# Optimization experiments

Measured on AMD Instinct MI355X. Metric: run time of the kernel, lower is better.

Reference implementation:

```python
import jax, jax.numpy as jnp
import numpy as np

B, D, Q, U = 4096, 512, 16384, 256  # batch, feat dim, CQ size, unique pids per batch
OIM_SCALAR = 30.0
IGNORE = -1


def _normalize(x):
    # F.normalize(dim=-1): divide by L2 norm clamped to eps
    n = jnp.maximum(jnp.linalg.norm(x, axis=-1, keepdims=True), 1e-12)
    return x / n


def setup_inputs() -> dict:
    key = jax.random.key(0)
    k1, k2, k3 = jax.random.split(key, 3)
    inputs = jax.random.normal(k1, (B, D), dtype=jnp.float32)
    # exactly U unique pids, each repeated B//U times, shuffled
    labels = jax.random.permutation(k2, jnp.arange(B, dtype=jnp.int32) % U)
    emb_cq = jax.random.normal(k3, (Q, D), dtype=jnp.float32)
    emb_cq = _normalize(emb_cq)  # queue stores normalized embeddings
    # unique queue labels; slice overlaps batch pids -> exercises the c==1 branch
    label_cq = jnp.arange(Q, dtype=jnp.int32) + 1000
    label_cq = label_cq.at[5000:5000 + U].set(jnp.arange(U, dtype=jnp.int32))
    age_cq = jnp.ones((Q,), dtype=jnp.int32)
    return {"inputs": inputs, "labels": labels, "emb_cq": emb_cq,
            "label_cq": label_cq, "age_cq": age_cq, "header_cq": 0}


def reference(inputs, labels, emb_cq, label_cq, age_cq, header_cq):
    # ---- per-pid masked mean (torch.unique loop, vectorized) ----
    uniq = jnp.unique(labels, size=U)                      # sorted unique pids [U]
    m_u = (uniq[:, None] == labels[None, :]).astype(inputs.dtype)  # [U,B]
    uniq_emb = (m_u @ inputs) / m_u.sum(axis=1, keepdims=True)     # [U,D]

    inputs_n = _normalize(inputs)
    uniq_emb_n = jax.lax.stop_gradient(_normalize(uniq_emb))  # queue write is under no_grad

    # ---- circular queue update (sequential, data-dependent) ----
    age_cq = age_cq + (label_cq != IGNORE).astype(age_cq.dtype)

    def step(carry, xy):
        emb, lab, age, h = carry
        x, y = xy
        m = lab == y
        c = m.any()
        i = jnp.argmax(m)          # existing slot for pid y (if any)
        emb = emb.at[h].set(x)
        lab = lab.at[h].set(y)
        age = age.at[h].set(1)
        inval = c & (i != h)       # invalidate stale slot
        lab = lab.at[i].set(jnp.where(inval, IGNORE, lab[i]))
        age = age.at[i].set(jnp.where(inval, 0, age[i]))
        return (emb, lab, age, (h + 1) % Q), None

    h0 = jnp.asarray(header_cq, dtype=jnp.int32)
    (emb_cq, label_cq, age_cq, _), _ = jax.lax.scan(
        step, (emb_cq, label_cq, age_cq, h0), (uniq_emb_n, uniq))
    emb_cq = jax.lax.stop_gradient(emb_cq)  # buffer: no grad through the queue

    # ---- cosine-sim cross-entropy over valid queue entries ----
    good = label_cq != IGNORE                               # [Q]
    # each batch pid matches exactly one good queue slot
    xe = jnp.argmax((labels[:, None] == label_cq[None, :]) & good[None, :], axis=1)
    logits = OIM_SCALAR * (inputs_n @ emb_cq.T)             # [B,Q]
    logits = jnp.where(good[None, :], logits, -jnp.inf)     # mask == compacting emb_cq[good]
    logp = jax.nn.log_softmax(logits, axis=1)
    loss = -jnp.mean(logp[jnp.arange(B), xe])               # sum(xe_i)/B
    return loss
```

## Files before the change

kernel.cpp:

```cpp
#include <hip/hip_runtime.h>
#include <hip/hip_bf16.h>

#define Bn 4096
#define Dn 512
#define Qn 16384
#define Un 256
#define OIM 30.0f


typedef int i32x4 __attribute__((ext_vector_type(4)));

__device__ __forceinline__ void async_copy16(const int4* g, int4* l) {
    __builtin_amdgcn_global_load_lds((const __attribute__((address_space(1))) void*)g,
                                     (__attribute__((address_space(3))) void*)l, 16, 0, 0);
}

__device__ __forceinline__ int clamp8(float v, float qs) {
    int q = __float2int_rn(v * qs);
    return max(-127, min(127, q));
}

__global__ void prep_kernel(const float* __restrict__ inputs, const int* __restrict__ labels,
                            const float* __restrict__ emb_cq, const int* __restrict__ label_cq,
                            const int* __restrict__ header,
                            char* __restrict__ inA8, char* __restrict__ embQ8,
                            float* __restrict__ invA, float* __restrict__ invB,
                            float* __restrict__ goodf, float* __restrict__ rowsum,
                            float* __restrict__ out) {
    __shared__ float wred[4];
    __shared__ float wmax[4];
    __shared__ int lidx[64];
    __shared__ int lcnt;
    int blk = blockIdx.x;
    int tid = threadIdx.x;
    float2 o;
    bool isA;
    int drow;
    if (blk == 0 && tid == 0) out[0] = 0.f;
    if (blk < Bn) {
        if (tid == 0) rowsum[blk] = 0.f;
        float2 v = ((const float2*)(inputs + (size_t)blk * Dn))[tid];
        float ss = v.x * v.x + v.y * v.y;
        for (int d = 1; d < 64; d <<= 1) ss += __shfl_xor(ss, d, 64);
        if ((tid & 63) == 0) wred[tid >> 6] = ss;
        __syncthreads();
        float sc = 1.0f / fmaxf(sqrtf(wred[0] + wred[1] + wred[2] + wred[3]), 1e-12f);
        o.x = v.x * sc; o.y = v.y * sc;
        isA = true; drow = blk;
    } else {
        int j = blk - Bn;
        int h0 = header[0];
        int t = j - h0; if (t < 0) t += Qn;
        if (t < Un) {
            if (tid == 0) lcnt = 0;
            __syncthreads();
            for (int b = tid; b < Bn; b += 256)
                if (labels[b] == t) { int s = atomicAdd(&lcnt, 1); if (s < 64) lidx[s] = b; }
            __syncthreads();
            int c = lcnt; if (c > 64) c = 64;
            float2 acc = {0.f, 0.f};
            for (int s = 0; s < c; ++s) {
                float2 x = ((const float2*)(inputs + (size_t)lidx[s] * Dn))[tid];
                acc.x += x.x; acc.y += x.y;
            }
            float inv = 1.0f / (float)(c > 0 ? c : 1);
            acc.x *= inv; acc.y *= inv;
            float ss = acc.x * acc.x + acc.y * acc.y;
            for (int d = 1; d < 64; d <<= 1) ss += __shfl_xor(ss, d, 64);
            if ((tid & 63) == 0) wred[tid >> 6] = ss;
            __syncthreads();
            float sc = 1.0f / fmaxf(sqrtf(wred[0] + wred[1] + wred[2] + wred[3]), 1e-12f);
            o.x = acc.x * sc; o.y = acc.y * sc;
        } else {
            o = ((const float2*)(emb_cq + (size_t)j * Dn))[tid];
        }
        if (tid == 0) {
            int vl = label_cq[j];
            int fin = (vl >= 0 && vl < Un) ? -1 : vl;
            if (t < Un) fin = t;
            goodf[j] = (fin != -1) ? 1.0f : 0.0f;
        }
        isA = false; drow = blk - Bn;
    }
    float am = fmaxf(fabsf(o.x), fabsf(o.y));
    for (int d = 1; d < 64; d <<= 1) am = fmaxf(am, __shfl_xor(am, d, 64));
    if ((tid & 63) == 0) wmax[tid >> 6] = am;
    __syncthreads();
    float m = fmaxf(fmaxf(fmaxf(wmax[0], wmax[1]), fmaxf(wmax[2], wmax[3])), 1e-12f);
    float qs = 127.0f / m;
    char2 pc;
    pc.x = (char)clamp8(o.x, qs);
    pc.y = (char)clamp8(o.y, qs);
    if (isA) {
        int kb = tid * 2;
        size_t addr = (size_t)(drow >> 4) * 8192 + (size_t)(kb >> 4) * 256
                    + (drow & 15) * 16 + (kb & 15);
        *(char2*)(inA8 + addr) = pc;
        if (tid == 0) invA[drow] = m / 127.0f;
    } else {
        *(char2*)(embQ8 + (size_t)drow * Dn + tid * 2) = pc;
        if (tid == 0) invB[drow] = m / 127.0f;
    }
}

__global__ __launch_bounds__(256, 4) void gemm_kernel(
    const char* __restrict__ inA8,
    const char* __restrict__ embQ8,
    const float* __restrict__ invA,
    const float* __restrict__ invB,
    const float* __restrict__ goodf,
    const int* __restrict__ labels,
    const int* __restrict__ header,
    float* __restrict__ rowsum,
    float* __restrict__ target)
{
    const float LOG2E = 1.4426950408889634f;
    const float LN2   = 0.6931471805599453f;
    __shared__ char Bs[4 * 128 * 64];
    __shared__ float rsl[128];
    __shared__ int tgtc[128];
    __shared__ float sAl[128];
    __shared__ float2 sBL[128];
    int tid = threadIdx.x;
    int lane = tid & 63, w = tid >> 6;
    int wm = w >> 1, wn = w & 1;
    int lid = blockIdx.y * gridDim.x + blockIdx.x;
    int xcd = lid & 7, pos = lid >> 3;
    int n0 = (xcd * 16 + (pos & 15)) * 128;
    int m0 = (pos >> 4) * 128;
    if (tid < 128) {
        rsl[tid] = 0.f;
        int tc = header[0] + labels[m0 + tid];
        if (tc >= Qn) tc -= Qn;
        tgtc[tid] = tc;
        sAl[tid] = invA[m0 + tid];
        float2 sb;
        sb.x = invB[n0 + tid];
        sb.y = (goodf[n0 + tid] != 0.f) ? 0.f : -10000.f;
        sBL[tid] = sb;
    }
    i32x4 acc[4][4] = {};
    const int4* Bg = (const int4*)(embQ8 + (size_t)n0 * Dn);
    int4* Bs4 = (int4*)Bs;
    int goff[2];
    #pragma unroll
    for (int t = 0; t < 2; ++t) {
        int g = t * 256 + tid;
        int r = g >> 2, sc = g & 3;
        int c = (sc - (r >> 1)) & 3;
        goff[t] = r * 32 + c;
    }
    int q = lane >> 4;
    int offB[4];
    #pragma unroll
    for (int j = 0; j < 4; ++j) {
        int br = wn * 64 + j * 16 + (lane & 15);
        offB[j] = br * 64 + (((q + (br >> 1)) & 3) << 4);
    }
    const char* Ap[4];
    #pragma unroll
    for (int i = 0; i < 4; ++i)
        Ap[i] = inA8 + (size_t)((m0 >> 4) + wm * 4 + i) * 8192 + lane * 16;
    auto stage2 = [&](int t) {
        int s0 = (t & 3) * 512, s1 = ((t + 1) & 3) * 512;
        #pragma unroll
        for (int u = 0; u < 2; ++u) {
            int g = u * 256 + tid;
            async_copy16(&Bg[goff[u] + t * 4],       &Bs4[s0 + g]);
            async_copy16(&Bg[goff[u] + (t + 1) * 4], &Bs4[s1 + g]);
        }
    };
    i32x4 a0[4], a1[4];
    auto loadA = [&](i32x4* a, int t) {
        #pragma unroll
        for (int i = 0; i < 4; ++i) a[i] = *(const i32x4*)(Ap[i] + t * 1024);
    };
    auto compute = [&](int t, i32x4* a) {
        const char* Bb = Bs + (t & 3) * 8192;
        i32x4 bfr[4];
        #pragma unroll
        for (int j = 0; j < 4; ++j) bfr[j] = *(const i32x4*)(Bb + offB[j]);
        #pragma unroll
        for (int i = 0; i < 4; ++i)
            #pragma unroll
            for (int j = 0; j < 4; ++j)
                acc[i][j] = __builtin_amdgcn_mfma_i32_16x16x64_i8(bfr[j], a[i], acc[i][j], 0, 0, 0);
    };
    stage2(0);
    loadA(a0, 0);
    #pragma unroll
    for (int ww = 0; ww < 8; ww += 2) {
        if (ww == 0)
            asm volatile("s_waitcnt vmcnt(4) lgkmcnt(0)\ns_barrier" ::: "memory");
        else
            asm volatile("s_waitcnt vmcnt(4)\ns_barrier" ::: "memory");
        loadA(a1, ww + 1);
        __builtin_amdgcn_sched_barrier(0);
        if (ww < 6) stage2(ww + 2);
        compute(ww, a0);
        if (ww < 6) loadA(a0, ww + 2);
        compute(ww + 1, a1);
    }
    int bl = lane & 15;
    float2 sbv[16];
    #pragma unroll
    for (int j = 0; j < 4; ++j)
        #pragma unroll
        for (int r = 0; r < 4; ++r)
            sbv[j * 4 + r] = sBL[wn * 64 + j * 16 + q * 4 + r];
    #pragma unroll
    for (int i = 0; i < 4; ++i) {
        int rowl = wm * 64 + i * 16 + bl;
        float fA = (OIM * LOG2E) * sAl[rowl];
        int tc = tgtc[rowl];
        float s = 0.f;
        #pragma unroll
        for (int j = 0; j < 4; ++j) {
            #pragma unroll
            for (int r = 0; r < 4; ++r) {
                int qloc = wn * 64 + j * 16 + q * 4 + r;
                float2 sb = sbv[j * 4 + r];
                float v2 = fA * sb.x * (float)acc[i][j][r] + sb.y;
                s += __builtin_amdgcn_exp2f(v2);
                if (tc == n0 + qloc) target[m0 + rowl] = v2 * LN2;
            }
        }
        s += __shfl_xor(s, 16, 64);
        s += __shfl_xor(s, 32, 64);
        if (q == 0) atomicAdd(&rsl[rowl], s);
    }
    __syncthreads();
    if (tid < 128) atomicAdd(&rowsum[m0 + tid], rsl[tid]);
}

__global__ void loss_kernel(const float* __restrict__ rowsum, const float* __restrict__ target,
                            float* __restrict__ out) {
    __shared__ float red[4];
    int tid = threadIdx.x;
    int b = blockIdx.x * 256 + tid;
    float s = logf(rowsum[b]) - target[b];
    #pragma unroll
    for (int d = 1; d < 64; d <<= 1) s += __shfl_xor(s, d, 64);
    if ((tid & 63) == 0) red[tid >> 6] = s;
    __syncthreads();
    if (tid == 0)
        atomicAdd(out, (red[0] + red[1] + red[2] + red[3]) * (1.0f / (float)Bn));
}

extern "C" void kernel_launch(void* const* d_in, const int* in_sizes, int n_in,
                              void* d_out, int out_size, void* d_ws, size_t ws_size,
                              hipStream_t stream) {
    const float* inputs   = (const float*)d_in[0];
    const int*   labels   = (const int*)d_in[1];
    const float* emb_cq   = (const float*)d_in[2];
    const int*   label_cq = (const int*)d_in[3];
    const int*   header   = (const int*)d_in[5];

    char* ws = (char*)d_ws;
    size_t off = 0;
    auto alloc = [&](size_t bytes) { char* p = ws + off; off += (bytes + 255) & ~(size_t)255; return p; };
    char*  inA8   = (char*)alloc((size_t)Bn * Dn);
    char*  embQ8  = (char*)alloc((size_t)Qn * Dn);
    float* invA   = (float*)alloc(Bn * 4);
    float* invB   = (float*)alloc(Qn * 4);
    float* goodf  = (float*)alloc(Qn * 4);
    float* rowsum = (float*)alloc(Bn * 4);
    float* target = (float*)alloc(Bn * 4);

    hipLaunchKernelGGL(prep_kernel, dim3(Bn + Qn), dim3(256), 0, stream,
                       inputs, labels, emb_cq, label_cq, header,
                       inA8, embQ8, invA, invB, goodf, rowsum, (float*)d_out);
    hipLaunchKernelGGL(gemm_kernel, dim3(Qn / 128, Bn / 128), dim3(256), 0, stream,
                       inA8, embQ8, invA, invB, goodf, labels, header, rowsum, target);
    hipLaunchKernelGGL(loss_kernel, dim3(Bn / 256), dim3(256), 0, stream,
                       rowsum, target, (float*)d_out);
}
```

Measured before the change: 169.9 us.

## Enlarge GEMM tile to 256x256 with 512 threads and 3-stage LDS pipeline

The int8 logits GEMM moves from 128x128 tiles with 256 threads to 256x256 tiles with 512 threads. The queue tile goes through a 3-slot LDS ring buffer with hand-tuned waitcnt values. MFMAs are issued in interleaved pairs under s_setprio, and LDS fragment loads are spread between MFMA groups. The goal is to halve global and LDS traffic per MFMA and hide load latency better. The cost is occupancy dropping to one block per CU, more accumulator registers, and a fused exp/target epilogue restructured around the new wave layout.

```diff
diff --git a/kernel.cpp b/kernel.cpp
--- a/kernel.cpp
+++ b/kernel.cpp
@@ -103,7 +103,46 @@
     }
 }
 
-__global__ __launch_bounds__(256, 4) void gemm_kernel(
+#define LDQ(T, K) (*(const i32x4*)(Bs + ((T) % 3) * 16384 + offQ[K]))
+#define STAGE2(T) do { int _sl = ((T) % 3) * 1024;                         \
+    async_copy16(&Bq[goff0 + (T) * 4], &Bs4[_sl + tid]);                   \
+    async_copy16(&Bq[goff1 + (T) * 4], &Bs4[_sl + 512 + tid]); } while (0)
+
+#define MFMA_PAIR(I0, I1, QA, QB, AF) do {                                 \
+    __builtin_amdgcn_s_setprio(1);                                         \
+    _Pragma("unroll")                                                      \
+    for (int j = 0; j < 4; ++j) {                                          \
+        acc[I0][j] = __builtin_amdgcn_mfma_i32_16x16x64_i8(QA, AF[j], acc[I0][j], 0, 0, 0); \
+        acc[I1][j] = __builtin_amdgcn_mfma_i32_16x16x64_i8(QB, AF[j], acc[I1][j], 0, 0, 0); \
+    }                                                                      \
+    __builtin_amdgcn_s_setprio(0);                                         \
+    __builtin_amdgcn_sched_barrier(0); } while (0)
+
+#define BODY(T, AFC, AFN) do {                                             \
+    __builtin_amdgcn_sched_barrier(0);                                     \
+    if ((T) == 0)      asm volatile("s_waitcnt vmcnt(2) lgkmcnt(0)");      \
+    else if ((T) <= 6) asm volatile("s_waitcnt vmcnt(6)");                 \
+    else               asm volatile("s_waitcnt vmcnt(4)");                 \
+    __builtin_amdgcn_s_barrier();                                          \
+    __builtin_amdgcn_sched_barrier(0);                                     \
+    i32x4 qA = LDQ(T, 0), qB = LDQ(T, 1);                                  \
+    if ((T) < 7) {                                                         \
+        _Pragma("unroll")                                                  \
+        for (int j = 0; j < 4; ++j)                                        \
+            AFN[j] = *(const i32x4*)(Ap[j] + ((T) + 1) * 1024);            \
+    }                                                                      \
+    __builtin_amdgcn_sched_barrier(0);                                     \
+    if ((T) < 6) STAGE2((T) + 2);                                          \
+    __builtin_amdgcn_sched_barrier(0);                                     \
+    i32x4 qC = LDQ(T, 2), qD = LDQ(T, 3);                                  \
+    MFMA_PAIR(0, 1, qA, qB, AFC);                                          \
+    i32x4 qE = LDQ(T, 4), qF = LDQ(T, 5);                                  \
+    MFMA_PAIR(2, 3, qC, qD, AFC);                                          \
+    i32x4 qG = LDQ(T, 6), qH = LDQ(T, 7);                                  \
+    MFMA_PAIR(4, 5, qE, qF, AFC);                                          \
+    MFMA_PAIR(6, 7, qG, qH, AFC); } while (0)
+
+__global__ __launch_bounds__(512, 1) void gemm_kernel(
     const char* __restrict__ inA8,
     const char* __restrict__ embQ8,
     const float* __restrict__ invA,
@@ -116,121 +155,94 @@
 {
     const float LOG2E = 1.4426950408889634f;
     const float LN2   = 0.6931471805599453f;
-    __shared__ char Bs[4 * 128 * 64];
-    __shared__ float rsl[128];
-    __shared__ int tgtc[128];
-    __shared__ float sAl[128];
-    __shared__ float2 sBL[128];
+    __shared__ char Bs[3 * 16384];
+    __shared__ float rsl[256];
+    __shared__ int tgt[256];
+    __shared__ float sAl[256];
+    __shared__ float2 sBL[256];
     int tid = threadIdx.x;
     int lane = tid & 63, w = tid >> 6;
-    int wm = w >> 1, wn = w & 1;
+    int wm = w >> 2, wn = w & 3;
     int lid = blockIdx.y * gridDim.x + blockIdx.x;
     int xcd = lid & 7, pos = lid >> 3;
-    int n0 = (xcd * 16 + (pos & 15)) * 128;
-    int m0 = (pos >> 4) * 128;
-    if (tid < 128) {
+    int q0 = (xcd * 8 + (pos & 7)) * 256;
+    int b0 = (pos >> 3) * 256;
+    if (tid < 256) {
         rsl[tid] = 0.f;
-        int tc = header[0] + labels[m0 + tid];
+        int tc = header[0] + labels[b0 + tid];
         if (tc >= Qn) tc -= Qn;
-        tgtc[tid] = tc;
-        sAl[tid] = invA[m0 + tid];
+        tgt[tid] = tc;
+        sAl[tid] = invA[b0 + tid];
         float2 sb;
-        sb.x = invB[n0 + tid];
-        sb.y = (goodf[n0 + tid] != 0.f) ? 0.f : -10000.f;
+        sb.x = invB[q0 + tid];
+        sb.y = (goodf[q0 + tid] != 0.f) ? 0.f : -10000.f;
         sBL[tid] = sb;
     }
-    i32x4 acc[4][4] = {};
-    const int4* Bg = (const int4*)(embQ8 + (size_t)n0 * Dn);
+    i32x4 acc[8][4] = {};
+    const int4* Bq = (const int4*)(embQ8 + (size_t)q0 * Dn);
     int4* Bs4 = (int4*)Bs;
-    int goff[2];
-    #pragma unroll
-    for (int t = 0; t < 2; ++t) {
-        int g = t * 256 + tid;
-        int r = g >> 2, sc = g & 3;
-        int c = (sc - (r >> 1)) & 3;
-        goff[t] = r * 32 + c;
-    }
-    int q = lane >> 4;
-    int offB[4];
+    int r0 = tid >> 2, sc0 = tid & 3;
+    int goff0 = r0 * 32 + ((sc0 - (r0 >> 1)) & 3);
+    int r1 = 128 + (tid >> 2);
+    int goff1 = r1 * 32 + ((sc0 - (r1 >> 1)) & 3);
+    int qq = lane >> 4;
+    int offQ[8];
+    #pragma unroll
+    for (int i = 0; i < 8; ++i) {
+        int r = wm * 128 + i * 16 + (lane & 15);
+        offQ[i] = r * 64 + (((qq + (r >> 1)) & 3) << 4);
+    }
+    const char* Ap[4];
+    #pragma unroll
+    for (int j = 0; j < 4; ++j)
+        Ap[j] = inA8 + (size_t)((b0 >> 4) + wn * 4 + j) * 8192 + lane * 16;
+    i32x4 af0[4], af1[4];
+    #pragma unroll
+    for (int j = 0; j < 4; ++j) af0[j] = *(const i32x4*)(Ap[j]);
+    __builtin_amdgcn_sched_barrier(0);
+    STAGE2(0);
+    STAGE2(1);
+    BODY(0, af0, af1);
+    BODY(1, af1, af0);
+    BODY(2, af0, af1);
+    BODY(3, af1, af0);
+    BODY(4, af0, af1);
+    BODY(5, af1, af0);
+    BODY(6, af0, af1);
+    BODY(7, af1, af0);
+    int bl = lane & 15;
+    float fAj[4]; int tcj[4]; float sj[4];
     #pragma unroll
     for (int j = 0; j < 4; ++j) {
-        int br = wn * 64 + j * 16 + (lane & 15);
-        offB[j] = br * 64 + (((q + (br >> 1)) & 3) << 4);
-    }
-    const char* Ap[4];
-    #pragma unroll
-    for (int i = 0; i < 4; ++i)
-        Ap[i] = inA8 + (size_t)((m0 >> 4) + wm * 4 + i) * 8192 + lane * 16;
-    auto stage2 = [&](int t) {
-        int s0 = (t & 3) * 512, s1 = ((t + 1) & 3) * 512;
+        int bcol = wn * 64 + j * 16 + bl;
+        fAj[j] = (OIM * LOG2E) * sAl[bcol];
+        tcj[j] = tgt[bcol];
+        sj[j] = 0.f;
+    }
+    #pragma unroll
+    for (int i = 0; i < 8; ++i) {
         #pragma unroll
-        for (int u = 0; u < 2; ++u) {
-            int g = u * 256 + tid;
-            async_copy16(&Bg[goff[u] + t * 4],       &Bs4[s0 + g]);
-            async_copy16(&Bg[goff[u] + (t + 1) * 4], &Bs4[s1 + g]);
-        }
-    };
-    i32x4 a0[4], a1[4];
-    auto loadA = [&](i32x4* a, int t) {
-        #pragma unroll
-        for (int i = 0; i < 4; ++i) a[i] = *(const i32x4*)(Ap[i] + t * 1024);
-    };
-    auto compute = [&](int t, i32x4* a) {
-        const char* Bb = Bs + (t & 3) * 8192;
-        i32x4 bfr[4];
-        #pragma unroll
-        for (int j = 0; j < 4; ++j) bfr[j] = *(const i32x4*)(Bb + offB[j]);
-        #pragma unroll
-        for (int i = 0; i < 4; ++i)
+        for (int r = 0; r < 4; ++r) {
+            int qloc = wm * 128 + i * 16 + qq * 4 + r;
+            float2 sb = sBL[qloc];
             #pragma unroll
-            for (int j = 0; j < 4; ++j)
-                acc[i][j] = __builtin_amdgcn_mfma_i32_16x16x64_i8(bfr[j], a[i], acc[i][j], 0, 0, 0);
-    };
-    stage2(0);
-    loadA(a0, 0);
-    #pragma unroll
-    for (int ww = 0; ww < 8; ww += 2) {
-        if (ww == 0)
-            asm volatile("s_waitcnt vmcnt(4) lgkmcnt(0)\ns_barrier" ::: "memory");
-        else
-            asm volatile("s_waitcnt vmcnt(4)\ns_barrier" ::: "memory");
-        loadA(a1, ww + 1);
-        __builtin_amdgcn_sched_barrier(0);
-        if (ww < 6) stage2(ww + 2);
-        compute(ww, a0);
-        if (ww < 6) loadA(a0, ww + 2);
-        compute(ww + 1, a1);
-    }
-    int bl = lane & 15;
-    float2 sbv[16];
-    #pragma unroll
-    for (int j = 0; j < 4; ++j)
-        #pragma unroll
-        for (int r = 0; r < 4; ++r)
-            sbv[j * 4 + r] = sBL[wn * 64 + j * 16 + q * 4 + r];
-    #pragma unroll
-    for (int i = 0; i < 4; ++i) {
-        int rowl = wm * 64 + i * 16 + bl;
-        float fA = (OIM * LOG2E) * sAl[rowl];
-        int tc = tgtc[rowl];
-        float s = 0.f;
-        #pragma unroll
-        for (int j = 0; j < 4; ++j) {
-            #pragma unroll
-            for (int r = 0; r < 4; ++r) {
-                int qloc = wn * 64 + j * 16 + q * 4 + r;
-                float2 sb = sbv[j * 4 + r];
-                float v2 = fA * sb.x * (float)acc[i][j][r] + sb.y;
-                s += __builtin_amdgcn_exp2f(v2);
-                if (tc == n0 + qloc) target[m0 + rowl] = v2 * LN2;
+            for (int j = 0; j < 4; ++j) {
+                float v2 = fAj[j] * sb.x * (float)acc[i][j][r] + sb.y;
+                sj[j] += __builtin_amdgcn_exp2f(v2);
+                if (tcj[j] == q0 + qloc)
+                    target[b0 + wn * 64 + j * 16 + bl] = v2 * LN2;
             }
         }
+    }
+    #pragma unroll
+    for (int j = 0; j < 4; ++j) {
+        float s = sj[j];
         s += __shfl_xor(s, 16, 64);
         s += __shfl_xor(s, 32, 64);
-        if (q == 0) atomicAdd(&rsl[rowl], s);
+        if (qq == 0) atomicAdd(&rsl[wn * 64 + j * 16 + bl], s);
     }
     __syncthreads();
-    if (tid < 128) atomicAdd(&rowsum[m0 + tid], rsl[tid]);
+    if (tid < 256) atomicAdd(&rowsum[b0 + tid], rsl[tid]);
 }
 
 __global__ void loss_kernel(const float* __restrict__ rowsum, const float* __restrict__ target,
@@ -270,7 +282,7 @@
     hipLaunchKernelGGL(prep_kernel, dim3(Bn + Qn), dim3(256), 0, stream,
                        inputs, labels, emb_cq, label_cq, header,
                        inA8, embQ8, invA, invB, goodf, rowsum, (float*)d_out);
-    hipLaunchKernelGGL(gemm_kernel, dim3(Qn / 128, Bn / 128), dim3(256), 0, stream,
+    hipLaunchKernelGGL(gemm_kernel, dim3(Qn / 256, Bn / 256), dim3(512), 0, stream,
                        inA8, embQ8, invA, invB, goodf, labels, header, rowsum, target);
     hipLaunchKernelGGL(loss_kernel, dim3(Bn / 256), dim3(256), 0, stream,
                        rowsum, target, (float*)d_out);
```

After: 158.6 us. 1.07x faster.
